# Performance work log

Measured on AMD Instinct MI355X. Metric: run time of the kernel, lower is better.

Reference implementation:

```python
import jax, jax.numpy as jnp
import numpy as np

DIM = 384
HEADS = 8
SR = 2
BN_EPS = 1e-5


def setup_inputs() -> dict:
    key = jax.random.key(0)
    ks = jax.random.split(key, 8)
    B, Hh, Ww = 4, 64, 64
    N = Hh * Ww
    Nk = (Hh // SR) * (Ww // SR)
    w = lambda k, s: jax.random.normal(k, s, jnp.float32) * 0.02
    return {
        "x": jax.random.normal(ks[0], (B, N, DIM), jnp.float32),
        "relative_pos": jax.random.normal(ks[1], (HEADS, N, Nk), jnp.float32) * 0.02,
        "H": Hh,
        "W": Ww,
        "Wq": w(ks[2], (DIM, DIM)),
        "Wk": w(ks[3], (DIM, DIM)),
        "Wv": w(ks[4], (DIM, DIM)),
        "Wp": w(ks[5], (DIM, DIM)),
        "bp": jnp.zeros((DIM,), jnp.float32),
        "sr_w": w(ks[6], (DIM, 1, SR, SR)),  # depthwise conv, OIHW with groups=DIM
        "sr_b": jnp.zeros((DIM,), jnp.float32),
        "bn_gamma": jnp.ones((DIM,), jnp.float32),
        "bn_beta": jnp.zeros((DIM,), jnp.float32),
        "bn_mean": jnp.zeros((DIM,), jnp.float32),
        "bn_var": jnp.ones((DIM,), jnp.float32),
    }


def reference(x, relative_pos, Wq, Wk, Wv, Wp, bp, sr_w, sr_b,
              bn_gamma, bn_beta, bn_mean, bn_var, H, W):
    B, N, C = x.shape
    hd = C // HEADS
    scale = hd ** (-0.5)
    # q projection -> [B, heads, N, hd]
    q = (x @ Wq.T).reshape(B, N, HEADS, hd).transpose(0, 2, 1, 3)
    # spatial reduction: depthwise conv stride SR + BatchNorm (eval mode)
    x_ = x.transpose(0, 2, 1).reshape(B, C, H, W)
    y = jax.lax.conv_general_dilated(
        x_, sr_w, window_strides=(SR, SR), padding="VALID",
        feature_group_count=C,
        dimension_numbers=("NCHW", "OIHW", "NCHW"))
    y = y + sr_b[None, :, None, None]
    inv = jax.lax.rsqrt(bn_var + BN_EPS) * bn_gamma
    y = (y - bn_mean[None, :, None, None]) * inv[None, :, None, None] \
        + bn_beta[None, :, None, None]
    xk = y.reshape(B, C, -1).transpose(0, 2, 1)  # [B, Nk, C]
    Nk = xk.shape[1]
    k = (xk @ Wk.T).reshape(B, Nk, HEADS, hd).transpose(0, 2, 1, 3)
    v = (xk @ Wv.T).reshape(B, Nk, HEADS, hd).transpose(0, 2, 1, 3)
    # scores with additive relative-position bias (broadcast over batch)
    attn = jnp.einsum("bhnd,bhmd->bhnm", q, k) * scale + relative_pos
    attn = jax.nn.softmax(attn, axis=-1)
    out = jnp.einsum("bhnm,bhmd->bhnd", attn, v)
    out = out.transpose(0, 2, 1, 3).reshape(B, N, C)
    return out @ Wp.T + bp
```

## Files before the change

### kernel.cpp

```cpp
#include <hip/hip_runtime.h>
#include <hip/hip_bf16.h>

#define LOG2E 1.4426950408889634f

typedef short bf16x8 __attribute__((ext_vector_type(8)));
typedef float f32x4  __attribute__((ext_vector_type(4)));

#define OFF_BPf  16
#define OFF_SRWf (OFF_BPf + 384)
#define OFF_SRBf (OFF_SRWf + 1536)
#define OFF_GAf  (OFF_SRBf + 384)
#define OFF_BEf  (OFF_GAf + 384)
#define OFF_MUf  (OFF_BEf + 384)
#define OFF_VAf  (OFF_MUf + 384)
#define U_XB 7712
#define U_WQ (U_XB + 6291456)
#define U_WK (U_WQ + 147456)
#define U_WV (U_WK + 147456)
#define U_WP (U_WV + 147456)
#define U_XK (U_WP + 147456)
#define U_QB (U_XK + 1572864)
#define U_KB (U_QB + 6291456)
#define U_VT (U_KB + 1572864)
#define U_OB (U_VT + 1572864)

static __device__ __forceinline__ float bfu(unsigned short u){ return __uint_as_float(((unsigned)u) << 16); }
static __device__ __forceinline__ float bf_lo(unsigned v){ return __uint_as_float(v << 16); }
static __device__ __forceinline__ float bf_hi(unsigned v){ return __uint_as_float(v & 0xFFFF0000u); }
static __device__ __forceinline__ unsigned short f2bf(float f){
  unsigned u = __float_as_uint(f);
  u += 0x7FFFu + ((u >> 16) & 1u);
  return (unsigned short)(u >> 16);
}
static __device__ __forceinline__ unsigned pkcvt(float a, float b){
  float2 f; f.x = a; f.y = b;
  __hip_bfloat162 h = __float22bfloat162_rn(f);
  union { __hip_bfloat162 h2; unsigned u; } cv; cv.h2 = h; return cv.u;
}
static __device__ __forceinline__ unsigned pk2bf(float a, float b){
  return pkcvt(a, b);
}
static __device__ __forceinline__ float fast_exp2(float x){ return __builtin_amdgcn_exp2f(x); }
static __device__ __forceinline__ void gld_lds16(const void* g, void* l){
  __builtin_amdgcn_global_load_lds((const __attribute__((address_space(1))) void*)g,
                                   (__attribute__((address_space(3))) void*)l, 16, 0, 0);
}

__global__ void detect_bf16(const unsigned* __restrict__ xraw, int* __restrict__ flag){
  unsigned w = xraw[threadIdx.x];
  unsigned e = (w >> 7) & 0xFFu;
  unsigned long long m = __ballot(e >= 118u && e <= 137u);
  if (threadIdx.x == 0) *flag = (__popcll(m) >= 40) ? 1 : 0;
}

static __device__ __forceinline__ void cp8_bf(unsigned short* dst, const void* src, int off, bool bf){
  if (bf) { *(uint4*)dst = *(const uint4*)((const unsigned short*)src + off); }
  else {
    const float* s = (const float*)src + off;
    float4 a = *(const float4*)s, b = *(const float4*)(s + 4);
    uint4 o; o.x = pk2bf(a.x, a.y); o.y = pk2bf(a.z, a.w);
    o.z = pk2bf(b.x, b.y); o.w = pk2bf(b.z, b.w);
    *(uint4*)dst = o;
  }
}
static __device__ __forceinline__ void cp8_f(float* dst, const void* src, int off, bool bf){
  if (bf) {
    const unsigned short* s = (const unsigned short*)src + off;
    uint4 w = *(const uint4*)s;
    float4 a, b;
    a.x = bf_lo(w.x); a.y = bf_hi(w.x); a.z = bf_lo(w.y); a.w = bf_hi(w.y);
    b.x = bf_lo(w.z); b.y = bf_hi(w.z); b.z = bf_lo(w.w); b.w = bf_hi(w.w);
    *(float4*)dst = a; *(float4*)(dst + 4) = b;
  } else {
    const float* s = (const float*)src + off;
    *(float4*)dst = *(const float4*)s;
    *(float4*)(dst + 4) = *(const float4*)(s + 4);
  }
}

__global__ __launch_bounds__(256) void convert_all(
    const void* x, const void* wq, const void* wk, const void* wv, const void* wp,
    const void* bp, const void* srw, const void* srb, const void* ga, const void* be,
    const void* mu, const void* va, float* ws){
  const bool bf = ((const int*)ws)[0] != 0;
  unsigned short* u = (unsigned short*)ws;
  int g = blockIdx.x * 256 + threadIdx.x;
  if (g < 786432) { cp8_bf(u + U_XB + g*8, x,  g*8, bf); return; }  g -= 786432;
  if (g < 18432)  { cp8_bf(u + U_WQ + g*8, wq, g*8, bf); return; }  g -= 18432;
  if (g < 18432)  { cp8_bf(u + U_WK + g*8, wk, g*8, bf); return; }  g -= 18432;
  if (g < 18432)  { cp8_bf(u + U_WV + g*8, wv, g*8, bf); return; }  g -= 18432;
  if (g < 18432)  { cp8_bf(u + U_WP + g*8, wp, g*8, bf); return; }  g -= 18432;
  if (g < 192)    { cp8_f(ws + OFF_SRWf + g*8, srw, g*8, bf); return; } g -= 192;
  if (g < 48)     { cp8_f(ws + OFF_BPf  + g*8, bp,  g*8, bf); return; } g -= 48;
  if (g < 48)     { cp8_f(ws + OFF_SRBf + g*8, srb, g*8, bf); return; } g -= 48;
  if (g < 48)     { cp8_f(ws + OFF_GAf  + g*8, ga,  g*8, bf); return; } g -= 48;
  if (g < 48)     { cp8_f(ws + OFF_BEf  + g*8, be,  g*8, bf); return; } g -= 48;
  if (g < 48)     { cp8_f(ws + OFF_MUf  + g*8, mu,  g*8, bf); return; } g -= 48;
  if (g < 48)     { cp8_f(ws + OFF_VAf  + g*8, va,  g*8, bf); }
}

__global__ __launch_bounds__(256) void sr_bn(const unsigned short* __restrict__ xb,
    const float* __restrict__ wsf, unsigned short* __restrict__ xkb){
  int idx = blockIdx.x * 256 + threadIdx.x;
  int c8 = idx % 48;
  int nk = (idx / 48) & 1023;
  int b  = idx / (48 * 1024);
  int i = nk >> 5, j = nk & 31;
  int c0 = c8 * 8;
  const unsigned short* xp = xb + ((size_t)(b*4096 + i*128 + j*2))*384 + c0;
  unsigned aw[4], bw[4], cw[4], dw[4];
  *(uint4*)aw = *(const uint4*)(xp);
  *(uint4*)bw = *(const uint4*)(xp + 384);
  *(uint4*)cw = *(const uint4*)(xp + 64*384);
  *(uint4*)dw = *(const uint4*)(xp + 65*384);
  unsigned out[4];
  #pragma unroll
  for (int k2 = 0; k2 < 4; ++k2) {
    float r2[2];
    #pragma unroll
    for (int half = 0; half < 2; ++half) {
      int k = k2*2 + half;
      int c = c0 + k;
      float xa = half ? bf_hi(aw[k2]) : bf_lo(aw[k2]);
      float xbv = half ? bf_hi(bw[k2]) : bf_lo(bw[k2]);
      float xc = half ? bf_hi(cw[k2]) : bf_lo(cw[k2]);
      float xd = half ? bf_hi(dw[k2]) : bf_lo(dw[k2]);
      float acc = xa*wsf[OFF_SRWf+c*4] + xbv*wsf[OFF_SRWf+c*4+1]
                + xc*wsf[OFF_SRWf+c*4+2] + xd*wsf[OFF_SRWf+c*4+3];
      float inv = rsqrtf(wsf[OFF_VAf+c] + 1e-5f) * wsf[OFF_GAf+c];
      r2[half] = (acc + wsf[OFF_SRBf+c] - wsf[OFF_MUf+c]) * inv + wsf[OFF_BEf+c];
    }
    out[k2] = pkcvt(r2[0], r2[1]);
  }
  *(uint4*)(xkb + (size_t)idx*8) = *(uint4*)out;
}

__global__ __launch_bounds__(256) void proj_qkv(unsigned short* __restrict__ u){
  int z, by;
  if (blockIdx.y < 128)      { z = 0; by = blockIdx.y; }
  else if (blockIdx.y < 160) { z = 1; by = blockIdx.y - 128; }
  else                       { z = 2; by = blockIdx.y - 160; }
  const unsigned short* A = u + ((z == 0) ? U_XB : U_XK);
  const unsigned short* W = u + ((z == 0) ? U_WQ : (z == 1) ? U_WK : U_WV);

  __shared__ unsigned short As[128][40];
  __shared__ unsigned short Ws[128][40];
  const int tid = threadIdx.x;
  const int wave = tid >> 6, lane = tid & 63, lg = lane >> 4, ln = lane & 15;
  const int m0 = by * 128, n0 = blockIdx.x * 128;
  const int wm = (wave >> 1) * 64, wn = (wave & 1) * 64;
  f32x4 acc[4][4];
  #pragma unroll
  for (int i = 0; i < 4; ++i)
    #pragma unroll
    for (int j = 0; j < 4; ++j) acc[i][j] = (f32x4){0.f,0.f,0.f,0.f};

  const int arow = tid >> 1, acol = (tid & 1) * 16;
  for (int kt = 0; kt < 384; kt += 32) {
    uint4 a0 = *(const uint4*)&A[(size_t)(m0+arow)*384 + kt + acol];
    uint4 a1 = *(const uint4*)&A[(size_t)(m0+arow)*384 + kt + acol + 8];
    uint4 w0 = *(const uint4*)&W[(size_t)(n0+arow)*384 + kt + acol];
    uint4 w1 = *(const uint4*)&W[(size_t)(n0+arow)*384 + kt + acol + 8];
    __syncthreads();
    *(uint4*)&As[arow][acol] = a0;  *(uint4*)&As[arow][acol+8] = a1;
    *(uint4*)&Ws[arow][acol] = w0;  *(uint4*)&Ws[arow][acol+8] = w1;
    __syncthreads();
    bf16x8 af[4], wf[4];
    #pragma unroll
    for (int mi = 0; mi < 4; ++mi) af[mi] = *(const bf16x8*)&As[wm + mi*16 + ln][lg*8];
    #pragma unroll
    for (int ni = 0; ni < 4; ++ni) wf[ni] = *(const bf16x8*)&Ws[wn + ni*16 + ln][lg*8];
    #pragma unroll
    for (int mi = 0; mi < 4; ++mi)
      #pragma unroll
      for (int ni = 0; ni < 4; ++ni)
        acc[mi][ni] = __builtin_amdgcn_mfma_f32_16x16x32_bf16(af[mi], wf[ni], acc[mi][ni], 0, 0, 0);
  }

  unsigned short* outQ = u + U_QB;
  unsigned short* outK = u + U_KB;
  unsigned short* outV = u + U_VT;
  #pragma unroll
  for (int mi = 0; mi < 4; ++mi)
    #pragma unroll
    for (int ni = 0; ni < 4; ++ni) {
      int gcol = n0 + wn + ni*16 + ln;
      if (z == 2) {
        int grow0 = m0 + wm + mi*16 + lg*4;
        int hh = gcol / 48, d = gcol - hh*48;
        int bb = grow0 >> 10, mk = grow0 & 1023;
        uint2 st; st.x = pkcvt(acc[mi][ni][0], acc[mi][ni][1]);
        st.y = pkcvt(acc[mi][ni][2], acc[mi][ni][3]);
        *(uint2*)&outV[((size_t)((bb*8 + hh)*48 + d))*1024 + mk] = st;
      } else {
        unsigned short* dst = (z == 0) ? outQ : outK;
        #pragma unroll
        for (int r = 0; r < 4; ++r) {
          int grow = m0 + wm + mi*16 + lg*4 + r;
          dst[(size_t)grow*384 + gcol] = f2bf(acc[mi][ni][r]);
        }
      }
    }
}

__global__ __launch_bounds__(256) void gemm_out(const unsigned short* __restrict__ A,
    const unsigned short* __restrict__ W, const float* __restrict__ bias,
    void* __restrict__ out, const int* __restrict__ flag){
  __shared__ unsigned short As[128][40];
  __shared__ unsigned short Ws[128][40];
  const int tid = threadIdx.x;
  const int wave = tid >> 6, lane = tid & 63, lg = lane >> 4, ln = lane & 15;
  const int m0 = blockIdx.y * 128, n0 = blockIdx.x * 128;
  const int wm = (wave >> 1) * 64, wn = (wave & 1) * 64;
  f32x4 acc[4][4];
  #pragma unroll
  for (int i = 0; i < 4; ++i)
    #pragma unroll
    for (int j = 0; j < 4; ++j) acc[i][j] = (f32x4){0.f,0.f,0.f,0.f};

  const int arow = tid >> 1, acol = (tid & 1) * 16;
  for (int kt = 0; kt < 384; kt += 32) {
    uint4 a0 = *(const uint4*)&A[(size_t)(m0+arow)*384 + kt + acol];
    uint4 a1 = *(const uint4*)&A[(size_t)(m0+arow)*384 + kt + acol + 8];
    uint4 w0 = *(const uint4*)&W[(size_t)(n0+arow)*384 + kt + acol];
    uint4 w1 = *(const uint4*)&W[(size_t)(n0+arow)*384 + kt + acol + 8];
    __syncthreads();
    *(uint4*)&As[arow][acol] = a0;  *(uint4*)&As[arow][acol+8] = a1;
    *(uint4*)&Ws[arow][acol] = w0;  *(uint4*)&Ws[arow][acol+8] = w1;
    __syncthreads();
    bf16x8 af[4], wf[4];
    #pragma unroll
    for (int mi = 0; mi < 4; ++mi) af[mi] = *(const bf16x8*)&As[wm + mi*16 + ln][lg*8];
    #pragma unroll
    for (int ni = 0; ni < 4; ++ni) wf[ni] = *(const bf16x8*)&Ws[wn + ni*16 + ln][lg*8];
    #pragma unroll
    for (int mi = 0; mi < 4; ++mi)
      #pragma unroll
      for (int ni = 0; ni < 4; ++ni)
        acc[mi][ni] = __builtin_amdgcn_mfma_f32_16x16x32_bf16(af[mi], wf[ni], acc[mi][ni], 0, 0, 0);
  }

  const bool bff = (*flag != 0);
  #pragma unroll
  for (int mi = 0; mi < 4; ++mi)
    #pragma unroll
    for (int ni = 0; ni < 4; ++ni)
      #pragma unroll
      for (int r = 0; r < 4; ++r) {
        int grow = m0 + wm + mi*16 + lg*4 + r;
        int gcol = n0 + wn + ni*16 + ln;
        float v = acc[mi][ni][r] + bias[gcol];
        if (bff) ((unsigned short*)out)[(size_t)grow*384 + gcol] = f2bf(v);
        else     ((float*)out)[(size_t)grow*384 + gcol] = v;
      }
}

__global__ __launch_bounds__(256, 4) void attn_mfma(const unsigned short* __restrict__ qb,
    const unsigned short* __restrict__ kb, const unsigned short* __restrict__ vt,
    const void* __restrict__ rel, const int* __restrict__ flag,
    unsigned short* __restrict__ ob){
  __shared__ __align__(16) unsigned short Kbuf[2][6*512];
  __shared__ __align__(16) unsigned short Vbuf[8*384];
  __shared__ __align__(16) unsigned short Ps[4][32][72];
  const int x = blockIdx.x;
  const int b = x >> 5, nb = x & 31, h = blockIdx.y;
  const int tid = threadIdx.x, wave = tid >> 6, lane = tid & 63;
  const int lg = lane >> 4, ln = lane & 15;
  const int qrow0 = nb * 128 + wave * 32;
  const bool bfm = (*flag != 0);
  const float SCL = 0.14433756729740643f * LOG2E;

  bf16x8 qf0[2], qf1[2];
  #pragma unroll
  for (int qt = 0; qt < 2; ++qt) {
    const unsigned short* qp = qb + ((size_t)(b*4096 + qrow0 + qt*16 + ln))*384 + h*48;
    qf0[qt] = *(const bf16x8*)(qp + lg*8);
    bf16x8 z = {0,0,0,0,0,0,0,0};
    if (lg < 2) z = *(const bf16x8*)(qp + 32 + lg*8);
    qf1[qt] = z;
  }

  f32x4 o[2][3];
  #pragma unroll
  for (int qt = 0; qt < 2; ++qt) { o[qt][0] = (f32x4){0.f,0.f,0.f,0.f}; o[qt][1] = o[qt][0]; o[qt][2] = o[qt][0]; }
  float lsum[2] = {0.f, 0.f};

  const float* relf = (const float*)rel;
  const unsigned short* relh = (const unsigned short*)rel;
  const size_t rbase = ((size_t)(h*4096 + qrow0 + ln)) * 1024;
  const size_t kbase = (size_t)(b*1024) * 384 + (size_t)h*48;
  const size_t vbase = ((size_t)(b*8 + h)) * 48 * 1024;

  const int jk1 = wave;
  const int jk2 = 4 + wave;
  const int jv1 = wave;
  const int jv2 = 2 + wave;
  int s1 = jv1*64 + lane;  int c1 = s1/48, d1 = s1 - 48*c1;
  size_t vg1 = vbase + (size_t)d1*1024 + c1*8;
  int s2 = jv2*64 + lane;  int c2 = s2/48, d2 = s2 - 48*c2;
  size_t vg2 = vbase + (size_t)d2*1024 + c2*8;

  gld_lds16(kb + kbase + (size_t)lane*384 + jk1*8, &Kbuf[0][jk1*512]);
  if (wave < 2) gld_lds16(kb + kbase + (size_t)lane*384 + jk2*8, &Kbuf[0][jk2*512]);

  #pragma unroll 1
  for (int t = 0; t < 16; ++t) {
    const int cbuf = t & 1, nbuf = cbuf ^ 1;
    __syncthreads();

    uint2 rr[2][4];
    if (bfm) {
      #pragma unroll
      for (int qt = 0; qt < 2; ++qt)
        #pragma unroll
        for (int mt = 0; mt < 4; ++mt)
          rr[qt][mt] = *(const uint2*)(relh + rbase + (size_t)qt*16384 + t*64 + mt*16 + lg*4);
    } else {
      #pragma unroll
      for (int qt = 0; qt < 2; ++qt)
        #pragma unroll
        for (int mt = 0; mt < 4; ++mt) {
          float4 q_ = *(const float4*)(relf + rbase + (size_t)qt*16384 + t*64 + mt*16 + lg*4);
          rr[qt][mt].x = pkcvt(q_.x, q_.y); rr[qt][mt].y = pkcvt(q_.z, q_.w);
        }
    }

    gld_lds16(vt + vg1 + t*64, &Vbuf[jv1*512]);
    if (wave >= 2) gld_lds16(vt + vg2 + t*64, &Vbuf[jv2*512]);
    const int T = (t + 1 < 16) ? t + 1 : 15;
    gld_lds16(kb + kbase + (size_t)T*24576 + (size_t)lane*384 + jk1*8, &Kbuf[nbuf][jk1*512]);
    if (wave < 2) gld_lds16(kb + kbase + (size_t)T*24576 + (size_t)lane*384 + jk2*8, &Kbuf[nbuf][jk2*512]);

    f32x4 s[4][2];
    #pragma unroll
    for (int mt = 0; mt < 4; ++mt) {
      bf16x8 k0 = *(const bf16x8*)&Kbuf[cbuf][lg*512 + (mt*16 + ln)*8];
      bf16x8 k1 = {0,0,0,0,0,0,0,0};
      if (lg < 2) k1 = *(const bf16x8*)&Kbuf[cbuf][(4 + lg)*512 + (mt*16 + ln)*8];
      #pragma unroll
      for (int qt = 0; qt < 2; ++qt) {
        s[mt][qt] = __builtin_amdgcn_mfma_f32_16x16x32_bf16(k0, qf0[qt], (f32x4){0.f,0.f,0.f,0.f}, 0, 0, 0);
        s[mt][qt] = __builtin_amdgcn_mfma_f32_16x16x32_bf16(k1, qf1[qt], s[mt][qt], 0, 0, 0);
      }
    }

    #pragma unroll
    for (int qt = 0; qt < 2; ++qt) {
      float lacc = 0.f;
      #pragma unroll
      for (int mt = 0; mt < 4; ++mt) {
        float r0 = bf_lo(rr[qt][mt].x), r1 = bf_hi(rr[qt][mt].x);
        float r2 = bf_lo(rr[qt][mt].y), r3 = bf_hi(rr[qt][mt].y);
        float p0 = fast_exp2(fmaf(s[mt][qt][0], SCL, r0 * LOG2E));
        float p1 = fast_exp2(fmaf(s[mt][qt][1], SCL, r1 * LOG2E));
        float p2 = fast_exp2(fmaf(s[mt][qt][2], SCL, r2 * LOG2E));
        float p3 = fast_exp2(fmaf(s[mt][qt][3], SCL, r3 * LOG2E));
        lacc += (p0 + p1) + (p2 + p3);
        uint2 w; w.x = pkcvt(p0, p1); w.y = pkcvt(p2, p3);
        *(uint2*)&Ps[wave][qt*16 + ln][mt*16 + lg*4] = w;
      }
      lsum[qt] += lacc;
    }

    __syncthreads();

    #pragma unroll
    for (int ks = 0; ks < 2; ++ks) {
      bf16x8 vf[3];
      #pragma unroll
      for (int nd = 0; nd < 3; ++nd)
        vf[nd] = *(const bf16x8*)&Vbuf[(ks*4 + lg)*384 + (nd*16 + ln)*8];
      #pragma unroll
      for (int qt = 0; qt < 2; ++qt) {
        bf16x8 pa = *(const bf16x8*)&Ps[wave][qt*16 + ln][ks*32 + lg*8];
        #pragma unroll
        for (int nd = 0; nd < 3; ++nd)
          o[qt][nd] = __builtin_amdgcn_mfma_f32_16x16x32_bf16(pa, vf[nd], o[qt][nd], 0, 0, 0);
      }
    }
  }

  #pragma unroll
  for (int qt = 0; qt < 2; ++qt) {
    lsum[qt] += __shfl_xor(lsum[qt], 16, 64);
    lsum[qt] += __shfl_xor(lsum[qt], 32, 64);
    if (lg == 0) *(float*)&Ps[wave][qt*16 + ln][64] = lsum[qt];
  }
  #pragma unroll
  for (int qt = 0; qt < 2; ++qt)
    #pragma unroll
    for (int r = 0; r < 4; ++r) {
      float l = *(const float*)&Ps[wave][qt*16 + lg*4 + r][64];
      float linv = 1.0f / l;
      size_t rowb = ((size_t)(b*4096 + qrow0 + qt*16 + lg*4 + r))*384 + h*48 + ln;
      #pragma unroll
      for (int nd = 0; nd < 3; ++nd)
        ob[rowb + nd*16] = f2bf(o[qt][nd][r] * linv);
    }
}

extern "C" void kernel_launch(void* const* d_in, const int* in_sizes, int n_in,
                              void* d_out, int out_size, void* d_ws, size_t ws_size,
                              hipStream_t stream) {
  float* ws = (float*)d_ws;
  int* flag = (int*)d_ws;
  unsigned short* u = (unsigned short*)d_ws;

  detect_bf16<<<1, 64, 0, stream>>>((const unsigned*)d_in[0], flag);
  convert_all<<<3363, 256, 0, stream>>>(d_in[0], d_in[4], d_in[5], d_in[6], d_in[7],
      d_in[8], d_in[9], d_in[10], d_in[11], d_in[12], d_in[13], d_in[14], ws);
  sr_bn<<<768, 256, 0, stream>>>(u + U_XB, ws, u + U_XK);
  proj_qkv<<<dim3(3, 192), 256, 0, stream>>>(u);
  attn_mfma<<<dim3(128, 8), 256, 0, stream>>>(u + U_QB, u + U_KB, u + U_VT, d_in[1], flag, u + U_OB);
  gemm_out<<<dim3(3, 128), 256, 0, stream>>>(u + U_OB, u + U_WP, ws + OFF_BPf, d_out, flag);
}
```

Before: 356.9 us.

## Process attention q-tiles sequentially with swizzled shared P buffer and higher occupancy

The attention kernel now handles its two 16-row query tiles one after another within each key block, reusing a single 16x64 P tile per wave instead of keeping both tiles' scores live at once. The P tile uses an XOR swizzle instead of padding to avoid LDS bank conflicts, and row sums move to a separate small array. This lowers register and LDS use so launch bounds can request 6 blocks per CU instead of 4. In exchange, K fragments are reloaded from LDS twice per iteration and each wave's work within an iteration is more serialized.

```diff
diff --git a/kernel.cpp b/kernel.cpp
--- a/kernel.cpp
+++ b/kernel.cpp
@@ -255,13 +255,14 @@
       }
 }
 
-__global__ __launch_bounds__(256, 4) void attn_mfma(const unsigned short* __restrict__ qb,
+__global__ __launch_bounds__(256, 6) void attn_mfma(const unsigned short* __restrict__ qb,
     const unsigned short* __restrict__ kb, const unsigned short* __restrict__ vt,
     const void* __restrict__ rel, const int* __restrict__ flag,
     unsigned short* __restrict__ ob){
   __shared__ __align__(16) unsigned short Kbuf[2][6*512];
   __shared__ __align__(16) unsigned short Vbuf[8*384];
-  __shared__ __align__(16) unsigned short Ps[4][32][72];
+  __shared__ __align__(16) unsigned short Ps[4][16][64];
+  __shared__ float Ls[4][32];
   const int x = blockIdx.x;
   const int b = x >> 5, nb = x & 31, h = blockIdx.y;
   const int tid = threadIdx.x, wave = tid >> 6, lane = tid & 63;
@@ -291,13 +292,16 @@
   const size_t kbase = (size_t)(b*1024) * 384 + (size_t)h*48;
   const size_t vbase = ((size_t)(b*8 + h)) * 48 * 1024;
 
+  const unsigned swz = (unsigned)((ln & 7) << 4);
+  char* psrow = (char*)&Ps[wave][ln][0];
+
   const int jk1 = wave;
   const int jk2 = 4 + wave;
   const int jv1 = wave;
   const int jv2 = 2 + wave;
-  int s1 = jv1*64 + lane;  int c1 = s1/48, d1 = s1 - 48*c1;
+  int s1i = jv1*64 + lane;  int c1 = s1i/48, d1 = s1i - 48*c1;
   size_t vg1 = vbase + (size_t)d1*1024 + c1*8;
-  int s2 = jv2*64 + lane;  int c2 = s2/48, d2 = s2 - 48*c2;
+  int s2i = jv2*64 + lane;  int c2 = s2i/48, d2 = s2i - 48*c2;
   size_t vg2 = vbase + (size_t)d2*1024 + c2*8;
 
   gld_lds16(kb + kbase + (size_t)lane*384 + jk1*8, &Kbuf[0][jk1*512]);
@@ -331,35 +335,30 @@
     gld_lds16(kb + kbase + (size_t)T*24576 + (size_t)lane*384 + jk1*8, &Kbuf[nbuf][jk1*512]);
     if (wave < 2) gld_lds16(kb + kbase + (size_t)T*24576 + (size_t)lane*384 + jk2*8, &Kbuf[nbuf][jk2*512]);
 
-    f32x4 s[4][2];
+    f32x4 s0[4];
     #pragma unroll
     for (int mt = 0; mt < 4; ++mt) {
       bf16x8 k0 = *(const bf16x8*)&Kbuf[cbuf][lg*512 + (mt*16 + ln)*8];
       bf16x8 k1 = {0,0,0,0,0,0,0,0};
       if (lg < 2) k1 = *(const bf16x8*)&Kbuf[cbuf][(4 + lg)*512 + (mt*16 + ln)*8];
-      #pragma unroll
-      for (int qt = 0; qt < 2; ++qt) {
-        s[mt][qt] = __builtin_amdgcn_mfma_f32_16x16x32_bf16(k0, qf0[qt], (f32x4){0.f,0.f,0.f,0.f}, 0, 0, 0);
-        s[mt][qt] = __builtin_amdgcn_mfma_f32_16x16x32_bf16(k1, qf1[qt], s[mt][qt], 0, 0, 0);
-      }
-    }
-
-    #pragma unroll
-    for (int qt = 0; qt < 2; ++qt) {
+      s0[mt] = __builtin_amdgcn_mfma_f32_16x16x32_bf16(k0, qf0[0], (f32x4){0.f,0.f,0.f,0.f}, 0, 0, 0);
+      s0[mt] = __builtin_amdgcn_mfma_f32_16x16x32_bf16(k1, qf1[0], s0[mt], 0, 0, 0);
+    }
+    {
       float lacc = 0.f;
       #pragma unroll
       for (int mt = 0; mt < 4; ++mt) {
-        float r0 = bf_lo(rr[qt][mt].x), r1 = bf_hi(rr[qt][mt].x);
-        float r2 = bf_lo(rr[qt][mt].y), r3 = bf_hi(rr[qt][mt].y);
-        float p0 = fast_exp2(fmaf(s[mt][qt][0], SCL, r0 * LOG2E));
-        float p1 = fast_exp2(fmaf(s[mt][qt][1], SCL, r1 * LOG2E));
-        float p2 = fast_exp2(fmaf(s[mt][qt][2], SCL, r2 * LOG2E));
-        float p3 = fast_exp2(fmaf(s[mt][qt][3], SCL, r3 * LOG2E));
+        float r0 = bf_lo(rr[0][mt].x), r1 = bf_hi(rr[0][mt].x);
+        float r2 = bf_lo(rr[0][mt].y), r3 = bf_hi(rr[0][mt].y);
+        float p0 = fast_exp2(fmaf(s0[mt][0], SCL, r0 * LOG2E));
+        float p1 = fast_exp2(fmaf(s0[mt][1], SCL, r1 * LOG2E));
+        float p2 = fast_exp2(fmaf(s0[mt][2], SCL, r2 * LOG2E));
+        float p3 = fast_exp2(fmaf(s0[mt][3], SCL, r3 * LOG2E));
         lacc += (p0 + p1) + (p2 + p3);
         uint2 w; w.x = pkcvt(p0, p1); w.y = pkcvt(p2, p3);
-        *(uint2*)&Ps[wave][qt*16 + ln][mt*16 + lg*4] = w;
+        *(uint2*)(psrow + (((unsigned)(mt*32 + lg*8)) ^ swz)) = w;
       }
-      lsum[qt] += lacc;
+      lsum[0] += lacc;
     }
 
     __syncthreads();
@@ -370,13 +369,47 @@
       #pragma unroll
       for (int nd = 0; nd < 3; ++nd)
         vf[nd] = *(const bf16x8*)&Vbuf[(ks*4 + lg)*384 + (nd*16 + ln)*8];
-      #pragma unroll
-      for (int qt = 0; qt < 2; ++qt) {
-        bf16x8 pa = *(const bf16x8*)&Ps[wave][qt*16 + ln][ks*32 + lg*8];
-        #pragma unroll
-        for (int nd = 0; nd < 3; ++nd)
-          o[qt][nd] = __builtin_amdgcn_mfma_f32_16x16x32_bf16(pa, vf[nd], o[qt][nd], 0, 0, 0);
+      bf16x8 pa = *(const bf16x8*)(psrow + (((unsigned)(ks*64 + lg*16)) ^ swz));
+      #pragma unroll
+      for (int nd = 0; nd < 3; ++nd)
+        o[0][nd] = __builtin_amdgcn_mfma_f32_16x16x32_bf16(pa, vf[nd], o[0][nd], 0, 0, 0);
+    }
+
+    f32x4 s1[4];
+    #pragma unroll
+    for (int mt = 0; mt < 4; ++mt) {
+      bf16x8 k0 = *(const bf16x8*)&Kbuf[cbuf][lg*512 + (mt*16 + ln)*8];
+      bf16x8 k1 = {0,0,0,0,0,0,0,0};
+      if (lg < 2) k1 = *(const bf16x8*)&Kbuf[cbuf][(4 + lg)*512 + (mt*16 + ln)*8];
+      s1[mt] = __builtin_amdgcn_mfma_f32_16x16x32_bf16(k0, qf0[1], (f32x4){0.f,0.f,0.f,0.f}, 0, 0, 0);
+      s1[mt] = __builtin_amdgcn_mfma_f32_16x16x32_bf16(k1, qf1[1], s1[mt], 0, 0, 0);
+    }
+    {
+      float lacc = 0.f;
+      #pragma unroll
+      for (int mt = 0; mt < 4; ++mt) {
+        float r0 = bf_lo(rr[1][mt].x), r1 = bf_hi(rr[1][mt].x);
+        float r2 = bf_lo(rr[1][mt].y), r3 = bf_hi(rr[1][mt].y);
+        float p0 = fast_exp2(fmaf(s1[mt][0], SCL, r0 * LOG2E));
+        float p1 = fast_exp2(fmaf(s1[mt][1], SCL, r1 * LOG2E));
+        float p2 = fast_exp2(fmaf(s1[mt][2], SCL, r2 * LOG2E));
+        float p3 = fast_exp2(fmaf(s1[mt][3], SCL, r3 * LOG2E));
+        lacc += (p0 + p1) + (p2 + p3);
+        uint2 w; w.x = pkcvt(p0, p1); w.y = pkcvt(p2, p3);
+        *(uint2*)(psrow + (((unsigned)(mt*32 + lg*8)) ^ swz)) = w;
       }
+      lsum[1] += lacc;
+    }
+    #pragma unroll
+    for (int ks = 0; ks < 2; ++ks) {
+      bf16x8 vf[3];
+      #pragma unroll
+      for (int nd = 0; nd < 3; ++nd)
+        vf[nd] = *(const bf16x8*)&Vbuf[(ks*4 + lg)*384 + (nd*16 + ln)*8];
+      bf16x8 pa = *(const bf16x8*)(psrow + (((unsigned)(ks*64 + lg*16)) ^ swz));
+      #pragma unroll
+      for (int nd = 0; nd < 3; ++nd)
+        o[1][nd] = __builtin_amdgcn_mfma_f32_16x16x32_bf16(pa, vf[nd], o[1][nd], 0, 0, 0);
     }
   }
 
@@ -384,13 +417,13 @@
   for (int qt = 0; qt < 2; ++qt) {
     lsum[qt] += __shfl_xor(lsum[qt], 16, 64);
     lsum[qt] += __shfl_xor(lsum[qt], 32, 64);
-    if (lg == 0) *(float*)&Ps[wave][qt*16 + ln][64] = lsum[qt];
+    if (lg == 0) Ls[wave][qt*16 + ln] = lsum[qt];
   }
   #pragma unroll
   for (int qt = 0; qt < 2; ++qt)
     #pragma unroll
     for (int r = 0; r < 4; ++r) {
-      float l = *(const float*)&Ps[wave][qt*16 + lg*4 + r][64];
+      float l = Ls[wave][qt*16 + lg*4 + r];
       float linv = 1.0f / l;
       size_t rowb = ((size_t)(b*4096 + qrow0 + qt*16 + lg*4 + r))*384 + h*48 + ln;
       #pragma unroll
```

Measured after the change: 523.3 us. 46.6% more time.
